# Kernel optimization log

Measured on AMD Instinct MI355X. Metric: run time of the kernel, lower is better.

## Reference

```python
import jax, jax.numpy as jnp
import numpy as np

B, C, H, W = 8, 64, 112, 112
KEY_NUM = 9


def conv1x1(x, w, b):
    # x: [b,c,h,w], w: [co,ci], b: [co]
    return jnp.einsum('bchw,oc->bohw', x, w) + b[None, :, None, None]


def bilinear_sample(feat, dy, dx):
    # feat: [b,c,H,W]; dy,dx: [b,H,W]. Zero-padded bilinear point sampling
    # (equivalent to torchvision deform_conv2d with 1x1 identity weight).
    b, c, h, w = feat.shape
    yy = jnp.arange(h, dtype=feat.dtype)[:, None]
    xx = jnp.arange(w, dtype=feat.dtype)[None, :]
    py = dy + yy  # [b,h,w]
    px = dx + xx
    y0 = jnp.floor(py)
    x0 = jnp.floor(px)
    wy1 = py - y0
    wx1 = px - x0
    wy0 = 1.0 - wy1
    wx0 = 1.0 - wx1
    featf = feat.reshape(b, c, h * w)

    def gather(yi, xi):
        valid = (yi >= 0) & (yi < h) & (xi >= 0) & (xi < w)
        yc = jnp.clip(yi, 0, h - 1).astype(jnp.int32)
        xc = jnp.clip(xi, 0, w - 1).astype(jnp.int32)
        idx = (yc * w + xc).reshape(b, 1, h * w)
        v = jnp.take_along_axis(featf, idx, axis=2).reshape(b, c, h, w)
        return v * valid.astype(feat.dtype)[:, None]

    return (gather(y0, x0) * (wy0 * wx0)[:, None]
            + gather(y0, x0 + 1) * (wy0 * wx1)[:, None]
            + gather(y0 + 1, x0) * (wy1 * wx0)[:, None]
            + gather(y0 + 1, x0 + 1) * (wy1 * wx1)[:, None])


def setup_inputs() -> dict:
    key = jax.random.key(0)
    ks = jax.random.split(key, 8)
    s = 1.0 / np.sqrt(C)
    return {
        'query_layer': jax.random.normal(ks[0], (B, C, H, W), jnp.float32),
        'key_layer': jax.random.normal(ks[1], (B, C, H, W), jnp.float32),
        'w_refer': jax.random.normal(ks[2], (C, C), jnp.float32) * s,
        'b_refer': jax.random.normal(ks[3], (C,), jnp.float32) * 0.1,
        'w_attn': jax.random.normal(ks[4], (KEY_NUM, C), jnp.float32) * s,
        'b_attn': jax.random.normal(ks[5], (KEY_NUM,), jnp.float32) * 0.1,
        'w_off': jax.random.normal(ks[6], (2 * KEY_NUM, C), jnp.float32) * s,
        'b_off': jax.random.normal(ks[7], (2 * KEY_NUM,), jnp.float32) * 0.1,
    }


def reference(query_layer, key_layer, w_refer, b_refer, w_attn, b_attn, w_off, b_off):
    key_feature = conv1x1(key_layer, w_refer, b_refer)          # [b,c,h,w]
    attn = jax.nn.softmax(conv1x1(query_layer, w_attn, b_attn), axis=1)  # [b,K,h,w]
    offset = conv1x1(query_layer, w_off, b_off)                  # [b,2K,h,w]
    # Faithful to original: key k uses offset channels [k, k+1] (overlapping slices)
    dys = jnp.moveaxis(offset[:, 0:KEY_NUM], 1, 0)               # [K,b,h,w]
    dxs = jnp.moveaxis(offset[:, 1:KEY_NUM + 1], 1, 0)           # [K,b,h,w]
    sampled = jax.vmap(bilinear_sample, in_axes=(None, 0, 0))(key_feature, dys, dxs)  # [K,b,c,h,w]
    out = jnp.einsum('kbchw,bkhw->bchw', sampled, attn)
    return out
```

## Files before the change

### kernel.cpp

```cpp
#include <hip/hip_runtime.h>

#define BB 8
#define CC 64
#define HH 112
#define WW 112
#define HWs (HH * WW)
#define KEYN 9

#define CK_PX 128
#define CK_TILES (HWs / CK_PX)
#define CK_NBLK (BB * CK_TILES)
#define WTS 68

#define SM_PX 32
#define SM_TILES (HWs / SM_PX)
#define SM_NBLK (BB * SM_TILES)

#define OFF_WQ   0
#define OFF_SB   1280
#define OFF_L    1300
#define OFF_P    0
#define OFF_OUTT 1972
#define SM_LDS   4148

__device__ __forceinline__ float swzx16(float v) {
    return __uint_as_float(__builtin_amdgcn_ds_swizzle(__float_as_uint(v), 0x401F));
}

__global__ __launch_bounds__(256, 3) void conv_key_kernel(
    const float* __restrict__ key, const float* __restrict__ w_refer,
    const float* __restrict__ b_refer, float* __restrict__ Kf)
{
    __shared__ float Xin[64 * CK_PX];
    __shared__ float Wt[64 * WTS];

    const int t = threadIdx.x;
    const int blk = blockIdx.x;
    const int b = blk / CK_TILES;
    const int s0 = (blk - b * CK_TILES) * CK_PX;
    const size_t inb = (size_t)b * CC * HWs + s0;

    #pragma unroll
    for (int m = 0; m < 4; ++m) {
        const int f = t + 256 * m;
        const int o = f >> 4;
        const int q = f & 15;
        const float4 wv = *reinterpret_cast<const float4*>(w_refer + o * CC + 4 * q);
        Wt[(4 * q + 0) * WTS + o] = wv.x;
        Wt[(4 * q + 1) * WTS + o] = wv.y;
        Wt[(4 * q + 2) * WTS + o] = wv.z;
        Wt[(4 * q + 3) * WTS + o] = wv.w;
    }
    #pragma unroll
    for (int m = 0; m < 8; ++m) {
        const int f = t + 256 * m;
        const int k = f >> 5;
        const int p8 = f & 31;
        *reinterpret_cast<float4*>(&Xin[k * CK_PX + 4 * p8]) =
            *reinterpret_cast<const float4*>(key + inb + (size_t)k * HWs + 4 * p8);
    }
    __syncthreads();

    const int og = t & 7;
    const int p4 = t >> 3;
    const float4 bias0 = *reinterpret_cast<const float4*>(b_refer + 8 * og);
    const float4 bias1 = *reinterpret_cast<const float4*>(b_refer + 8 * og + 4);
    float4 acc[4][2];
    #pragma unroll
    for (int pi = 0; pi < 4; ++pi) { acc[pi][0] = bias0; acc[pi][1] = bias1; }

    #pragma unroll 4
    for (int k = 0; k < 64; ++k) {
        const float4 a4 = *reinterpret_cast<const float4*>(&Xin[k * CK_PX + 4 * p4]);
        const float4 w0 = *reinterpret_cast<const float4*>(&Wt[k * WTS + 8 * og]);
        const float4 w1 = *reinterpret_cast<const float4*>(&Wt[k * WTS + 8 * og + 4]);
        const float ap[4] = {a4.x, a4.y, a4.z, a4.w};
        #pragma unroll
        for (int pi = 0; pi < 4; ++pi) {
            acc[pi][0].x = fmaf(ap[pi], w0.x, acc[pi][0].x);
            acc[pi][0].y = fmaf(ap[pi], w0.y, acc[pi][0].y);
            acc[pi][0].z = fmaf(ap[pi], w0.z, acc[pi][0].z);
            acc[pi][0].w = fmaf(ap[pi], w0.w, acc[pi][0].w);
            acc[pi][1].x = fmaf(ap[pi], w1.x, acc[pi][1].x);
            acc[pi][1].y = fmaf(ap[pi], w1.y, acc[pi][1].y);
            acc[pi][1].z = fmaf(ap[pi], w1.z, acc[pi][1].z);
            acc[pi][1].w = fmaf(ap[pi], w1.w, acc[pi][1].w);
        }
    }

    #pragma unroll
    for (int pi = 0; pi < 4; ++pi) {
        const size_t ob = ((size_t)b * HWs + s0 + 4 * p4 + pi) * CC + 8 * og;
        *reinterpret_cast<float4*>(Kf + ob)     = acc[pi][0];
        *reinterpret_cast<float4*>(Kf + ob + 4) = acc[pi][1];
    }
}

__global__ __launch_bounds__(256, 8) void fused_sample_kernel(
    const float* __restrict__ query, const float* __restrict__ w_attn,
    const float* __restrict__ b_attn, const float* __restrict__ w_off,
    const float* __restrict__ b_off, const float* __restrict__ Kf,
    float* __restrict__ out)
{
    __shared__ float S[SM_LDS];
    float*  Wq   = S + OFF_WQ;
    float*  Sb   = S + OFF_SB;
    float*  L    = S + OFF_L;
    float4* Pf   = reinterpret_cast<float4*>(S + OFF_P);
    float*  OutT = S + OFF_OUTT;

    const int t = threadIdx.x;
    const int l = t & 63;
    const int w = t >> 6;
    const int blk = blockIdx.x;
    const int b = blk & 7;
    const int tile = blk >> 3;
    const int s0 = tile * SM_PX;
    const size_t qb = (size_t)b * CC * HWs + s0;
    const char* Kfb = reinterpret_cast<const char*>(Kf) + (size_t)b * HWs * CC * 4;

    for (int f = t; f < 304; f += 256) {
        const int r = f >> 4;
        const int q = f & 15;
        const float* src = (r < KEYN) ? (w_attn + r * CC) : (w_off + (r - KEYN) * CC);
        const float4 wv = *reinterpret_cast<const float4*>(src + 4 * q);
        Wq[(4 * q + 0) * 20 + r] = wv.x;
        Wq[(4 * q + 1) * 20 + r] = wv.y;
        Wq[(4 * q + 2) * 20 + r] = wv.z;
        Wq[(4 * q + 3) * 20 + r] = wv.w;
    }
    if (t < 64) Wq[t * 20 + 19] = 0.f;
    if (t < 20) Sb[t] = (t < KEYN) ? b_attn[t] : (t < 19 ? b_off[t - KEYN] : 0.f);
    __syncthreads();

    {
        const int px = t & 31;
        const int og = t >> 5;
        if (og < 5) {
            const int o4 = 4 * og;
            float4 acc = *reinterpret_cast<const float4*>(&Sb[o4]);
            #pragma unroll 8
            for (int k = 0; k < 64; ++k) {
                const float a = query[qb + (size_t)k * HWs + px];
                const float4 wv = *reinterpret_cast<const float4*>(&Wq[k * 20 + o4]);
                acc.x = fmaf(a, wv.x, acc.x);
                acc.y = fmaf(a, wv.y, acc.y);
                acc.z = fmaf(a, wv.z, acc.z);
                acc.w = fmaf(a, wv.w, acc.w);
            }
            L[px * 21 + o4 + 0] = acc.x;
            L[px * 21 + o4 + 1] = acc.y;
            L[px * 21 + o4 + 2] = acc.z;
            L[px * 21 + o4 + 3] = acc.w;
        }
    }
    __syncthreads();

    if (t < SM_PX) {
        float lg[KEYN], of[10];
        #pragma unroll
        for (int k = 0; k < KEYN; ++k) lg[k] = L[t * 21 + k];
        #pragma unroll
        for (int j = 0; j < 10; ++j) of[j] = L[t * 21 + KEYN + j];
        float m = lg[0];
        #pragma unroll
        for (int k = 1; k < KEYN; ++k) m = fmaxf(m, lg[k]);
        float s = 0.f, e[KEYN];
        #pragma unroll
        for (int k = 0; k < KEYN; ++k) { e[k] = expf(lg[k] - m); s += e[k]; }
        const float sinv = 1.0f / s;
        #pragma unroll
        for (int k = 0; k < KEYN; ++k)
            Pf[t * KEYN + k] = make_float4(e[k] * sinv, of[k], of[k + 1], 0.f);
    }
    __syncthreads();

    const int sub  = l >> 5;
    const int c2   = (l >> 4) & 1;
    const int cb16 = (l & 15) * 16;
    const float fc2 = (float)c2;

    for (int j = 0; j < 4; ++j) {
        const int p = w * 8 + 2 * j + sub;
        const int s = s0 + p;
        const int y = s / WW;
        const int x = s - y * WW;
        const float4* Pp = Pf + p * KEYN;

        float4 acc0 = make_float4(0.f, 0.f, 0.f, 0.f);
        float4 acc1 = make_float4(0.f, 0.f, 0.f, 0.f);
        #pragma unroll
        for (int k = 0; k < KEYN; ++k) {
            const float4 pk = Pp[k];
            const float py  = pk.y + (float)y;
            const float pxx = pk.z + (float)x;
            const float fy = floorf(py), fx = floorf(pxx);
            const float wy1 = py - fy, wx1 = pxx - fx;
            const int ix = (int)fx + c2;
            const int xc = min(max(ix, 0), WW - 1);
            const float vx = (ix >= 0 && ix < WW) ? 1.f : 0.f;
            const float wx = (fc2 * wx1 + (1.f - fc2) * (1.f - wx1)) * vx * pk.x;
            const int iy0 = (int)fy, iy1 = iy0 + 1;
            const int yc0 = min(max(iy0, 0), HH - 1);
            const int yc1 = min(max(iy1, 0), HH - 1);
            const float w0 = ((iy0 >= 0 && iy0 < HH) ? 1.f : 0.f) * (1.f - wy1) * wx;
            const float w1 = ((iy1 >= 0 && iy1 < HH) ? 1.f : 0.f) * wy1 * wx;
            const unsigned a0 = (unsigned)((yc0 * WW + xc) * (CC * 4)) + cb16;
            const unsigned a1 = (unsigned)((yc1 * WW + xc) * (CC * 4)) + cb16;
            const float4 v0 = *reinterpret_cast<const float4*>(Kfb + a0);
            const float4 v1 = *reinterpret_cast<const float4*>(Kfb + a1);
            acc0.x = fmaf(v0.x, w0, acc0.x); acc0.y = fmaf(v0.y, w0, acc0.y);
            acc0.z = fmaf(v0.z, w0, acc0.z); acc0.w = fmaf(v0.w, w0, acc0.w);
            acc1.x = fmaf(v1.x, w1, acc1.x); acc1.y = fmaf(v1.y, w1, acc1.y);
            acc1.z = fmaf(v1.z, w1, acc1.z); acc1.w = fmaf(v1.w, w1, acc1.w);
        }
        float4 acc;
        acc.x = acc0.x + acc1.x; acc.y = acc0.y + acc1.y;
        acc.z = acc0.z + acc1.z; acc.w = acc0.w + acc1.w;

        acc.x += swzx16(acc.x); acc.y += swzx16(acc.y);
        acc.z += swzx16(acc.z); acc.w += swzx16(acc.w);

        if ((l & 16) == 0) {
            float* d = OutT + p * 68 + (cb16 >> 2);
            *reinterpret_cast<float4*>(d) = acc;
        }
    }
    __syncthreads();

    const size_t ob = (size_t)b * CC * HWs + s0;
    #pragma unroll
    for (int m = 0; m < 8; ++m) {
        const int f = t + 256 * m;
        const int c = f >> 5;
        const int px = f & 31;
        out[ob + (size_t)c * HWs + px] = OutT[px * 68 + c];
    }
}

extern "C" void kernel_launch(void* const* d_in, const int* in_sizes, int n_in,
                              void* d_out, int out_size, void* d_ws, size_t ws_size,
                              hipStream_t stream)
{
    const float* query   = (const float*)d_in[0];
    const float* key     = (const float*)d_in[1];
    const float* w_refer = (const float*)d_in[2];
    const float* b_refer = (const float*)d_in[3];
    const float* w_attn  = (const float*)d_in[4];
    const float* b_attn  = (const float*)d_in[5];
    const float* w_off   = (const float*)d_in[6];
    const float* b_off   = (const float*)d_in[7];
    float* out = (float*)d_out;

    float* Kf = (float*)d_ws;

    hipLaunchKernelGGL(conv_key_kernel, dim3(CK_NBLK), dim3(256), 0, stream,
                       key, w_refer, b_refer, Kf);
    hipLaunchKernelGGL(fused_sample_kernel, dim3(SM_NBLK), dim3(256), 0, stream,
                       query, w_attn, b_attn, w_off, b_off, Kf, out);
}
```

Before: 162.2 us.

## Precompute bilinear sample addresses and weights once per tile in LDS

Stages the query tile into shared memory with vectorized float4 loads, so the per-pixel 1x1 conv reads LDS instead of issuing strided scalar global loads. Adds a pass that computes each (pixel, key, x-corner) gather address pair and bilinear weights once into an LDS table. Before, all 16 lanes per pixel redundantly recomputed this address and weight math inside the sampling loop. The cost is a larger LDS footprint, an extra barrier, and a transposed parameter layout.

```diff
diff --git a/kernel.cpp b/kernel.cpp
--- a/kernel.cpp
+++ b/kernel.cpp
@@ -19,9 +19,11 @@
 #define OFF_WQ   0
 #define OFF_SB   1280
 #define OFF_L    1300
+#define OFF_XQ   1972
 #define OFF_P    0
-#define OFF_OUTT 1972
-#define SM_LDS   4148
+#define OFF_T    0
+#define OFF_OUTT 2304
+#define SM_LDS   4480
 
 __device__ __forceinline__ float swzx16(float v) {
     return __uint_as_float(__builtin_amdgcn_ds_swizzle(__float_as_uint(v), 0x401F));
@@ -96,6 +98,42 @@
     }
 }
 
+__device__ __forceinline__ float4 make_entry(int e, float4 pk, int s0)
+{
+    const int px = e & 31;
+    const int c2 = (e >> 5) & 1;
+    const int s = s0 + px;
+    const int yi = s / WW;
+    const int xi = s - yi * WW;
+    const float py  = pk.y + (float)yi;
+    const float pxf = pk.z + (float)xi;
+    const float fy = floorf(py), fx = floorf(pxf);
+    const float wy1 = py - fy, wx1 = pxf - fx;
+    const int ix = (int)fx + c2;
+    const int xc = min(max(ix, 0), WW - 1);
+    const float vx = (ix >= 0 && ix < WW) ? 1.f : 0.f;
+    const float wxc = (c2 ? wx1 : (1.f - wx1)) * vx * pk.x;
+    const int iy0 = (int)fy;
+    const int iy1 = iy0 + 1;
+    const int yc0 = min(max(iy0, 0), HH - 1);
+    const int yc1 = min(max(iy1, 0), HH - 1);
+    const float w0 = ((iy0 >= 0 && iy0 < HH) ? 1.f : 0.f) * (1.f - wy1) * wxc;
+    const float w1 = ((iy1 >= 0 && iy1 < HH) ? 1.f : 0.f) * wy1 * wxc;
+    const unsigned a0 = (unsigned)((yc0 * WW + xc) * (CC * 4));
+    const unsigned a1 = (unsigned)((yc1 * WW + xc) * (CC * 4));
+    float4 r;
+    r.x = __uint_as_float(a0);
+    r.y = __uint_as_float(a1);
+    r.z = w0;
+    r.w = w1;
+    return r;
+}
+
+__device__ __forceinline__ int twidx(int e)
+{
+    return ((e >> 6) << 6) + ((e & 31) << 1) + ((e >> 5) & 1);
+}
+
 __global__ __launch_bounds__(256, 8) void fused_sample_kernel(
     const float* __restrict__ query, const float* __restrict__ w_attn,
     const float* __restrict__ b_attn, const float* __restrict__ w_off,
@@ -106,7 +144,9 @@
     float*  Wq   = S + OFF_WQ;
     float*  Sb   = S + OFF_SB;
     float*  L    = S + OFF_L;
-    float4* Pf   = reinterpret_cast<float4*>(S + OFF_P);
+    float*  Xq   = S + OFF_XQ;
+    float4* Pf4  = reinterpret_cast<float4*>(S + OFF_P);
+    float4* Tf4  = reinterpret_cast<float4*>(S + OFF_T);
     float*  OutT = S + OFF_OUTT;
 
     const int t = threadIdx.x;
@@ -131,6 +171,14 @@
     }
     if (t < 64) Wq[t * 20 + 19] = 0.f;
     if (t < 20) Sb[t] = (t < KEYN) ? b_attn[t] : (t < 19 ? b_off[t - KEYN] : 0.f);
+    #pragma unroll
+    for (int m = 0; m < 2; ++m) {
+        const int f = t + 256 * m;
+        const int c = f >> 3;
+        const int p4 = (f & 7) * 4;
+        *reinterpret_cast<float4*>(&Xq[c * 32 + p4]) =
+            *reinterpret_cast<const float4*>(query + qb + (size_t)c * HWs + p4);
+    }
     __syncthreads();
 
     {
@@ -141,7 +189,7 @@
             float4 acc = *reinterpret_cast<const float4*>(&Sb[o4]);
             #pragma unroll 8
             for (int k = 0; k < 64; ++k) {
-                const float a = query[qb + (size_t)k * HWs + px];
+                const float a = Xq[k * 32 + px];
                 const float4 wv = *reinterpret_cast<const float4*>(&Wq[k * 20 + o4]);
                 acc.x = fmaf(a, wv.x, acc.x);
                 acc.y = fmaf(a, wv.y, acc.y);
@@ -171,48 +219,44 @@
         const float sinv = 1.0f / s;
         #pragma unroll
         for (int k = 0; k < KEYN; ++k)
-            Pf[t * KEYN + k] = make_float4(e[k] * sinv, of[k], of[k + 1], 0.f);
+            Pf4[k * 32 + t] = make_float4(e[k] * sinv, of[k], of[k + 1], 0.f);
+    }
+    __syncthreads();
+
+    {
+        const int px = t & 31;
+        const float4 q0 = Pf4[((t      ) >> 6) * 32 + px];
+        const float4 q1 = Pf4[((t + 256) >> 6) * 32 + px];
+        float4 q2 = make_float4(0.f, 0.f, 0.f, 0.f);
+        if (t < 64) q2 = Pf4[((t + 512) >> 6) * 32 + px];
+        __syncthreads();
+        Tf4[twidx(t)]       = make_entry(t,       q0, s0);
+        Tf4[twidx(t + 256)] = make_entry(t + 256, q1, s0);
+        if (t < 64) Tf4[twidx(t + 512)] = make_entry(t + 512, q2, s0);
     }
     __syncthreads();
 
     const int sub  = l >> 5;
     const int c2   = (l >> 4) & 1;
     const int cb16 = (l & 15) * 16;
-    const float fc2 = (float)c2;
 
     for (int j = 0; j < 4; ++j) {
         const int p = w * 8 + 2 * j + sub;
-        const int s = s0 + p;
-        const int y = s / WW;
-        const int x = s - y * WW;
-        const float4* Pp = Pf + p * KEYN;
+        const float4* Tp = Tf4 + p * 2 + c2;
 
         float4 acc0 = make_float4(0.f, 0.f, 0.f, 0.f);
         float4 acc1 = make_float4(0.f, 0.f, 0.f, 0.f);
         #pragma unroll
         for (int k = 0; k < KEYN; ++k) {
-            const float4 pk = Pp[k];
-            const float py  = pk.y + (float)y;
-            const float pxx = pk.z + (float)x;
-            const float fy = floorf(py), fx = floorf(pxx);
-            const float wy1 = py - fy, wx1 = pxx - fx;
-            const int ix = (int)fx + c2;
-            const int xc = min(max(ix, 0), WW - 1);
-            const float vx = (ix >= 0 && ix < WW) ? 1.f : 0.f;
-            const float wx = (fc2 * wx1 + (1.f - fc2) * (1.f - wx1)) * vx * pk.x;
-            const int iy0 = (int)fy, iy1 = iy0 + 1;
-            const int yc0 = min(max(iy0, 0), HH - 1);
-            const int yc1 = min(max(iy1, 0), HH - 1);
-            const float w0 = ((iy0 >= 0 && iy0 < HH) ? 1.f : 0.f) * (1.f - wy1) * wx;
-            const float w1 = ((iy1 >= 0 && iy1 < HH) ? 1.f : 0.f) * wy1 * wx;
-            const unsigned a0 = (unsigned)((yc0 * WW + xc) * (CC * 4)) + cb16;
-            const unsigned a1 = (unsigned)((yc1 * WW + xc) * (CC * 4)) + cb16;
+            const float4 tv = Tp[k * 64];
+            const unsigned a0 = __float_as_uint(tv.x) + cb16;
+            const unsigned a1 = __float_as_uint(tv.y) + cb16;
             const float4 v0 = *reinterpret_cast<const float4*>(Kfb + a0);
             const float4 v1 = *reinterpret_cast<const float4*>(Kfb + a1);
-            acc0.x = fmaf(v0.x, w0, acc0.x); acc0.y = fmaf(v0.y, w0, acc0.y);
-            acc0.z = fmaf(v0.z, w0, acc0.z); acc0.w = fmaf(v0.w, w0, acc0.w);
-            acc1.x = fmaf(v1.x, w1, acc1.x); acc1.y = fmaf(v1.y, w1, acc1.y);
-            acc1.z = fmaf(v1.z, w1, acc1.z); acc1.w = fmaf(v1.w, w1, acc1.w);
+            acc0.x = fmaf(v0.x, tv.z, acc0.x); acc0.y = fmaf(v0.y, tv.z, acc0.y);
+            acc0.z = fmaf(v0.z, tv.z, acc0.z); acc0.w = fmaf(v0.w, tv.z, acc0.w);
+            acc1.x = fmaf(v1.x, tv.w, acc1.x); acc1.y = fmaf(v1.y, tv.w, acc1.y);
+            acc1.z = fmaf(v1.z, tv.w, acc1.z); acc1.w = fmaf(v1.w, tv.w, acc1.w);
         }
         float4 acc;
         acc.x = acc0.x + acc1.x; acc.y = acc0.y + acc1.y;
```

Measured after the change: 151.9 us. 6.4% less time.
